# Kernel optimization log

Measured on AMD Instinct MI355X. Metric: run time of the kernel, lower is better.

## Reference

```python
import jax, jax.numpy as jnp
import numpy as np

EPS = 1e-8
MASK_MIN = 0.0


def setup_inputs() -> dict:
    key = jax.random.key(0)
    k1, k2, k3, k4 = jax.random.split(key, 4)
    B, H, CELLS, W = 8, 8, 8192, 256
    memory = jax.random.normal(k1, (B, CELLS, W), dtype=jnp.float32)
    keys = jax.random.normal(k2, (B, H, W), dtype=jnp.float32)
    betas = jax.random.uniform(k3, (B, H), dtype=jnp.float32)
    mask = jax.random.uniform(k4, (B, H, W), dtype=jnp.float32)
    return {"memory": memory, "keys": keys, "betas": betas, "mask": mask}


def reference(memory, keys, betas, mask):
    # memory: [B, C, W]; keys: [B, H, W]; betas: [B, H]; mask: [B, H, W]
    mask = mask * (1.0 - MASK_MIN) + MASK_MIN
    m2 = mask * mask                                   # [B, H, W]
    keys_m = keys * mask                               # masked keys
    # (memory*mask) . (keys*mask) summed over W == memory . (keys*mask^2)
    dots = jnp.einsum('bcw,bhw->bhc', memory, keys * m2)        # [B, H, C]
    keys_norm = jnp.linalg.norm(keys_m, axis=-1)                # [B, H]
    mem_norm = jnp.sqrt(jnp.einsum('bcw,bhw->bhc', memory * memory, m2))  # [B, H, C]
    norm = keys_norm[..., None] * mem_norm                      # [B, H, C]
    scores = dots / (norm + EPS) * betas[..., None]
    return jax.nn.softmax(scores, axis=-1)                      # [B, H, C]
```

## Files before the change

kernel.cpp:

```cpp
#include <hip/hip_runtime.h>
#include <cstdint>
#include <cmath>

#define EPS_F 1e-8f

constexpr int B = 8, H = 8, CELLS = 8192, W = 256;
constexpr int W4 = 64;
constexpr int TC = 32;
constexpr int NBLK = CELLS / TC;
constexpr int PAD = 65;

__global__ __launch_bounds__(256, 3) void ca_scores(
    const float4* __restrict__ mem4,
    const float* __restrict__ keys,
    const float* __restrict__ mask,
    const float* __restrict__ betas,
    float* __restrict__ out,
    float2* __restrict__ part)
{
    __shared__ float4 s_tile[TC * PAD];
    __shared__ float4 s_kq[H * PAD];
    __shared__ float4 s_m2[H * PAD];
    __shared__ float  s_kn[H];
    __shared__ float  s_fin[4 * H];
    __shared__ float  s_sum[4 * H];
    __shared__ float  s_sc[H][TC + 1];

    const int b = blockIdx.y, blk = blockIdx.x, t = threadIdx.x;
    const int c0 = blk * TC;
    const int lane = t & 63, wv = t >> 6;

    const int ph = t >> 5;
    const int pw = t & 31;
    const float4* __restrict__ kb4 = (const float4*)(keys + ((size_t)b * H + ph) * W);
    const float4* __restrict__ mb4 = (const float4*)(mask + ((size_t)b * H + ph) * W);
    float4 k0 = kb4[pw], k1 = kb4[pw + 32];
    float4 m0 = mb4[pw], m1 = mb4[pw + 32];

    const float4* __restrict__ gbase = mem4 + ((size_t)b * CELLS + c0) * W4;
    float4 st[8];
#pragma unroll
    for (int i = 0; i < 8; ++i) st[i] = gbase[t + i * 256];

    float4 q0 = make_float4(m0.x * m0.x, m0.y * m0.y, m0.z * m0.z, m0.w * m0.w);
    float4 q1 = make_float4(m1.x * m1.x, m1.y * m1.y, m1.z * m1.z, m1.w * m1.w);
    float4 kq0 = make_float4(k0.x * q0.x, k0.y * q0.y, k0.z * q0.z, k0.w * q0.w);
    float4 kq1 = make_float4(k1.x * q1.x, k1.y * q1.y, k1.z * q1.z, k1.w * q1.w);
    s_kq[ph * PAD + pw]      = kq0;
    s_kq[ph * PAD + pw + 32] = kq1;
    s_m2[ph * PAD + pw]      = q0;
    s_m2[ph * PAD + pw + 32] = q1;
    float km;
    float v = 0.f;
    km = k0.x * m0.x; v = fmaf(km, km, v);
    km = k0.y * m0.y; v = fmaf(km, km, v);
    km = k0.z * m0.z; v = fmaf(km, km, v);
    km = k0.w * m0.w; v = fmaf(km, km, v);
    km = k1.x * m1.x; v = fmaf(km, km, v);
    km = k1.y * m1.y; v = fmaf(km, km, v);
    km = k1.z * m1.z; v = fmaf(km, km, v);
    km = k1.w * m1.w; v = fmaf(km, km, v);
#pragma unroll
    for (int s = 1; s < 32; s <<= 1) v += __shfl_xor(v, s, 64);
    if ((t & 31) == 0) s_kn[ph] = sqrtf(v);

#pragma unroll
    for (int i = 0; i < 8; ++i) {
        int g = t + i * 256;
        s_tile[(g >> 6) * PAD + (g & 63)] = st[i];
    }
    __syncthreads();

    const int h  = lane & 7;
    const int cs = lane >> 3;
    const int c  = wv * 8 + cs;
    const float4* __restrict__ pa = s_tile + c * PAD;
    const float4* __restrict__ pk = s_kq + h * PAD;
    const float4* __restrict__ pq = s_m2 + h * PAD;

    float4 dt = make_float4(0.f, 0.f, 0.f, 0.f);
    float4 nr = make_float4(0.f, 0.f, 0.f, 0.f);
#pragma unroll 8
    for (int w = 0; w < W4; ++w) {
        float4 a  = pa[w];
        float4 kq = pk[w];
        float4 q  = pq[w];
        dt.x = fmaf(a.x, kq.x, dt.x);
        dt.y = fmaf(a.y, kq.y, dt.y);
        dt.z = fmaf(a.z, kq.z, dt.z);
        dt.w = fmaf(a.w, kq.w, dt.w);
        nr.x = fmaf(a.x * a.x, q.x, nr.x);
        nr.y = fmaf(a.y * a.y, q.y, nr.y);
        nr.z = fmaf(a.z * a.z, q.z, nr.z);
        nr.w = fmaf(a.w * a.w, q.w, nr.w);
    }
    float d = (dt.x + dt.y) + (dt.z + dt.w);
    float n = (nr.x + nr.y) + (nr.z + nr.w);

    float kn = s_kn[h];
    float be = betas[b * H + h];
    float score = d * be / (kn * sqrtf(n) + EPS_F);
    s_sc[h][c] = score;

    float mx = score;
#pragma unroll
    for (int s = 8; s < 64; s <<= 1) mx = fmaxf(mx, __shfl_xor(mx, s, 64));
    if (lane < 8) s_fin[wv * 8 + lane] = mx;
    __syncthreads();

    {
        const int oh = t >> 5, oc = t & 31;
        out[((size_t)(b * H + oh)) * CELLS + c0 + oc] = s_sc[oh][oc];
    }
    float gm = fmaxf(fmaxf(s_fin[h], s_fin[8 + h]),
                     fmaxf(s_fin[16 + h], s_fin[24 + h]));
    float e = expf(score - gm);
#pragma unroll
    for (int s = 8; s < 64; s <<= 1) e += __shfl_xor(e, s, 64);
    if (lane < 8) s_sum[wv * 8 + lane] = e;
    __syncthreads();
    if (t < 8) {
        float s4 = (s_sum[t] + s_sum[8 + t]) + (s_sum[16 + t] + s_sum[24 + t]);
        part[((size_t)(b * H + t)) * NBLK + blk] = make_float2(gm, s4);
    }
}

__global__ __launch_bounds__(256) void ca_norm(
    float* __restrict__ out, const float2* __restrict__ part)
{
    const int row = blockIdx.x >> 3;
    const int seg = blockIdx.x & 7;
    const int t = threadIdx.x, lane = t & 63;

    const float2* __restrict__ pp = part + (size_t)row * NBLK;
    float2 a0 = pp[lane], a1 = pp[lane + 64], a2 = pp[lane + 128], a3 = pp[lane + 192];
    float gm = fmaxf(fmaxf(a0.x, a1.x), fmaxf(a2.x, a3.x));
#pragma unroll
    for (int s = 32; s; s >>= 1) gm = fmaxf(gm, __shfl_xor(gm, s, 64));
    float gs = a0.y * expf(a0.x - gm) + a1.y * expf(a1.x - gm)
             + a2.y * expf(a2.x - gm) + a3.y * expf(a3.x - gm);
#pragma unroll
    for (int s = 32; s; s >>= 1) gs += __shfl_xor(gs, s, 64);
    float inv = 1.0f / gs;

    float4* p = (float4*)(out + (size_t)row * CELLS) + seg * 256;
    float4 vv = p[t];
    vv.x = expf(vv.x - gm) * inv;
    vv.y = expf(vv.y - gm) * inv;
    vv.z = expf(vv.z - gm) * inv;
    vv.w = expf(vv.w - gm) * inv;
    p[t] = vv;
}

extern "C" void kernel_launch(void* const* d_in, const int* in_sizes, int n_in,
                              void* d_out, int out_size, void* d_ws, size_t ws_size,
                              hipStream_t stream) {
    (void)in_sizes; (void)n_in; (void)out_size; (void)ws_size;
    const float* memory = (const float*)d_in[0];
    const float* keys   = (const float*)d_in[1];
    const float* betas  = (const float*)d_in[2];
    const float* mask   = (const float*)d_in[3];
    float* out = (float*)d_out;
    float2* part = (float2*)d_ws;

    dim3 gA(NBLK, B);
    ca_scores<<<gA, 256, 0, stream>>>((const float4*)memory, keys, mask, betas,
                                      out, part);
    ca_norm<<<8 * B * H, 256, 0, stream>>>(out, part);
}
```

Measured before the change: 28.27 us.

## Precompute masked keys in prep kernel and hold them in registers with DPP reductions

Adds a small prep kernel that computes keys*mask^2, mask^2, key norms and betas once per (b,h) and writes them to workspace in a lane-friendly interleaved layout. The score kernel then loads these weights straight into registers instead of rebuilding them in shared memory in every block. Each lane covers two heads and a slice of W across 8 cells, and the partial sums are reduced with DPP row rotations. This is meant to cut redundant per-block key/mask work and shared-memory reads. In exchange it adds a third kernel launch and raises register pressure to 16 float4 weights per thread.

```diff
diff --git a/kernel.cpp b/kernel.cpp
--- a/kernel.cpp
+++ b/kernel.cpp
@@ -8,121 +8,148 @@
 constexpr int W4 = 64;
 constexpr int TC = 32;
 constexpr int NBLK = CELLS / TC;
-constexpr int PAD = 65;
+
+constexpr int OFF_CB   = 32768;
+constexpr int OFF_PART = 32896;
+
+template <int CTRL>
+__device__ __forceinline__ float ror_add(float v) {
+    int x = __builtin_amdgcn_update_dpp(0, __builtin_bit_cast(int, v),
+                                        CTRL, 0xf, 0xf, false);
+    return v + __builtin_bit_cast(float, x);
+}
+__device__ __forceinline__ float row_sum16(float v) {
+    v = ror_add<0x121>(v);
+    v = ror_add<0x122>(v);
+    v = ror_add<0x124>(v);
+    v = ror_add<0x128>(v);
+    return v;
+}
+
+__global__ __launch_bounds__(256) void ca_prep(
+    const float* __restrict__ keys, const float* __restrict__ mask,
+    const float* __restrict__ betas, float* __restrict__ ws)
+{
+    const int bh = blockIdx.x;
+    const int b = bh >> 3, h = bh & 7;
+    const int t = threadIdx.x;
+    float k = keys[bh * W + t];
+    float m = mask[bh * W + t];
+    float m2 = m * m;
+    float kq = k * m2;
+
+    const int w4 = t >> 2, e = t & 3;
+    const int j = w4 >> 4, wsl = w4 & 15;
+    const int hp = h & 3, hh = h >> 2;
+    size_t base = ((((size_t)b * 64 + hp * 16 + wsl) * 16) + j * 4 + hh * 2) * 4 + e;
+    ws[base]     = kq;
+    ws[base + 4] = m2;
+
+    float km = k * m;
+    float v = km * km;
+#pragma unroll
+    for (int s = 32; s; s >>= 1) v += __shfl_xor(v, s, 64);
+    __shared__ float red[4];
+    const int lane = t & 63, wv = t >> 6;
+    if (lane == 0) red[wv] = v;
+    __syncthreads();
+    if (t == 0) {
+        float kn = sqrtf((red[0] + red[1]) + (red[2] + red[3]));
+        ((float2*)(ws + OFF_CB))[bh] = make_float2(kn, betas[bh]);
+    }
+}
 
 __global__ __launch_bounds__(256, 3) void ca_scores(
     const float4* __restrict__ mem4,
-    const float* __restrict__ keys,
-    const float* __restrict__ mask,
-    const float* __restrict__ betas,
+    const float* __restrict__ ws,
     float* __restrict__ out,
     float2* __restrict__ part)
 {
-    __shared__ float4 s_tile[TC * PAD];
-    __shared__ float4 s_kq[H * PAD];
-    __shared__ float4 s_m2[H * PAD];
-    __shared__ float  s_kn[H];
-    __shared__ float  s_fin[4 * H];
-    __shared__ float  s_sum[4 * H];
+    __shared__ float4 s_tile[TC * W4];
     __shared__ float  s_sc[H][TC + 1];
+    __shared__ float  s_fin[H], s_sum2[H];
 
     const int b = blockIdx.y, blk = blockIdx.x, t = threadIdx.x;
     const int c0 = blk * TC;
     const int lane = t & 63, wv = t >> 6;
-
-    const int ph = t >> 5;
-    const int pw = t & 31;
-    const float4* __restrict__ kb4 = (const float4*)(keys + ((size_t)b * H + ph) * W);
-    const float4* __restrict__ mb4 = (const float4*)(mask + ((size_t)b * H + ph) * W);
-    float4 k0 = kb4[pw], k1 = kb4[pw + 32];
-    float4 m0 = mb4[pw], m1 = mb4[pw + 32];
+    const int hp  = (lane >> 4) & 3;
+    const int wsl = lane & 15;
 
     const float4* __restrict__ gbase = mem4 + ((size_t)b * CELLS + c0) * W4;
     float4 st[8];
 #pragma unroll
     for (int i = 0; i < 8; ++i) st[i] = gbase[t + i * 256];
 
-    float4 q0 = make_float4(m0.x * m0.x, m0.y * m0.y, m0.z * m0.z, m0.w * m0.w);
-    float4 q1 = make_float4(m1.x * m1.x, m1.y * m1.y, m1.z * m1.z, m1.w * m1.w);
-    float4 kq0 = make_float4(k0.x * q0.x, k0.y * q0.y, k0.z * q0.z, k0.w * q0.w);
-    float4 kq1 = make_float4(k1.x * q1.x, k1.y * q1.y, k1.z * q1.z, k1.w * q1.w);
-    s_kq[ph * PAD + pw]      = kq0;
-    s_kq[ph * PAD + pw + 32] = kq1;
-    s_m2[ph * PAD + pw]      = q0;
-    s_m2[ph * PAD + pw + 32] = q1;
-    float km;
-    float v = 0.f;
-    km = k0.x * m0.x; v = fmaf(km, km, v);
-    km = k0.y * m0.y; v = fmaf(km, km, v);
-    km = k0.z * m0.z; v = fmaf(km, km, v);
-    km = k0.w * m0.w; v = fmaf(km, km, v);
-    km = k1.x * m1.x; v = fmaf(km, km, v);
-    km = k1.y * m1.y; v = fmaf(km, km, v);
-    km = k1.z * m1.z; v = fmaf(km, km, v);
-    km = k1.w * m1.w; v = fmaf(km, km, v);
+    const float4* __restrict__ tbase = (const float4*)ws + ((size_t)b * 64 + lane) * 16;
+    float4 tb[16];
 #pragma unroll
-    for (int s = 1; s < 32; s <<= 1) v += __shfl_xor(v, s, 64);
-    if ((t & 31) == 0) s_kn[ph] = sqrtf(v);
+    for (int i = 0; i < 16; ++i) tb[i] = tbase[i];
+    const float2* __restrict__ cbp = (const float2*)(ws + OFF_CB) + b * H;
+    float2 cbA = cbp[hp];
+    float2 cbB = cbp[hp + 4];
 
 #pragma unroll
-    for (int i = 0; i < 8; ++i) {
-        int g = t + i * 256;
-        s_tile[(g >> 6) * PAD + (g & 63)] = st[i];
+    for (int i = 0; i < 8; ++i) s_tile[t + i * 256] = st[i];
+    __syncthreads();
+
+#pragma unroll
+    for (int c = 0; c < 8; ++c) {
+        const int cell = wv * 8 + c;
+        const float4* __restrict__ pr = s_tile + cell * W4 + wsl;
+        float4 a0 = pr[0], a1 = pr[16], a2 = pr[32], a3 = pr[48];
+
+        float4 dA = make_float4(0.f, 0.f, 0.f, 0.f);
+        float4 nA = make_float4(0.f, 0.f, 0.f, 0.f);
+        float4 dB = make_float4(0.f, 0.f, 0.f, 0.f);
+        float4 nB = make_float4(0.f, 0.f, 0.f, 0.f);
+
+#define ACC(a, j)                                                           \
+        {                                                                   \
+            float4 sq = make_float4(a.x * a.x, a.y * a.y, a.z * a.z, a.w * a.w); \
+            float4 kqA = tb[(j) * 4 + 0], qA = tb[(j) * 4 + 1];             \
+            float4 kqB = tb[(j) * 4 + 2], qB = tb[(j) * 4 + 3];             \
+            dA.x = fmaf(a.x, kqA.x, dA.x); dA.y = fmaf(a.y, kqA.y, dA.y);   \
+            dA.z = fmaf(a.z, kqA.z, dA.z); dA.w = fmaf(a.w, kqA.w, dA.w);   \
+            nA.x = fmaf(sq.x, qA.x, nA.x); nA.y = fmaf(sq.y, qA.y, nA.y);   \
+            nA.z = fmaf(sq.z, qA.z, nA.z); nA.w = fmaf(sq.w, qA.w, nA.w);   \
+            dB.x = fmaf(a.x, kqB.x, dB.x); dB.y = fmaf(a.y, kqB.y, dB.y);   \
+            dB.z = fmaf(a.z, kqB.z, dB.z); dB.w = fmaf(a.w, kqB.w, dB.w);   \
+            nB.x = fmaf(sq.x, qB.x, nB.x); nB.y = fmaf(sq.y, qB.y, nB.y);   \
+            nB.z = fmaf(sq.z, qB.z, nB.z); nB.w = fmaf(sq.w, qB.w, nB.w);   \
+        }
+        ACC(a0, 0) ACC(a1, 1) ACC(a2, 2) ACC(a3, 3)
+#undef ACC
+
+        float d0 = (dA.x + dA.y) + (dA.z + dA.w);
+        float n0 = (nA.x + nA.y) + (nA.z + nA.w);
+        float d1 = (dB.x + dB.y) + (dB.z + dB.w);
+        float n1 = (nB.x + nB.y) + (nB.z + nB.w);
+        d0 = row_sum16(d0); n0 = row_sum16(n0);
+        d1 = row_sum16(d1); n1 = row_sum16(n1);
+
+        float s0 = d0 * cbA.y / (cbA.x * sqrtf(n0) + EPS_F);
+        float s1 = d1 * cbB.y / (cbB.x * sqrtf(n1) + EPS_F);
+        if (wsl == c) {
+            s_sc[hp][cell]     = s0;
+            s_sc[hp + 4][cell] = s1;
+        }
     }
     __syncthreads();
 
-    const int h  = lane & 7;
-    const int cs = lane >> 3;
-    const int c  = wv * 8 + cs;
-    const float4* __restrict__ pa = s_tile + c * PAD;
-    const float4* __restrict__ pk = s_kq + h * PAD;
-    const float4* __restrict__ pq = s_m2 + h * PAD;
+    const int oh = t >> 5, oc = t & 31;
+    float sc = s_sc[oh][oc];
+    out[((size_t)(b * H + oh)) * CELLS + c0 + oc] = sc;
 
-    float4 dt = make_float4(0.f, 0.f, 0.f, 0.f);
-    float4 nr = make_float4(0.f, 0.f, 0.f, 0.f);
-#pragma unroll 8
-    for (int w = 0; w < W4; ++w) {
-        float4 a  = pa[w];
-        float4 kq = pk[w];
-        float4 q  = pq[w];
-        dt.x = fmaf(a.x, kq.x, dt.x);
-        dt.y = fmaf(a.y, kq.y, dt.y);
-        dt.z = fmaf(a.z, kq.z, dt.z);
-        dt.w = fmaf(a.w, kq.w, dt.w);
-        nr.x = fmaf(a.x * a.x, q.x, nr.x);
-        nr.y = fmaf(a.y * a.y, q.y, nr.y);
-        nr.z = fmaf(a.z * a.z, q.z, nr.z);
-        nr.w = fmaf(a.w * a.w, q.w, nr.w);
-    }
-    float d = (dt.x + dt.y) + (dt.z + dt.w);
-    float n = (nr.x + nr.y) + (nr.z + nr.w);
-
-    float kn = s_kn[h];
-    float be = betas[b * H + h];
-    float score = d * be / (kn * sqrtf(n) + EPS_F);
-    s_sc[h][c] = score;
-
-    float mx = score;
+    float mx = sc;
 #pragma unroll
-    for (int s = 8; s < 64; s <<= 1) mx = fmaxf(mx, __shfl_xor(mx, s, 64));
-    if (lane < 8) s_fin[wv * 8 + lane] = mx;
+    for (int s = 1; s <= 16; s <<= 1) mx = fmaxf(mx, __shfl_xor(mx, s, 64));
+    float e = expf(sc - mx);
+#pragma unroll
+    for (int s = 1; s <= 16; s <<= 1) e += __shfl_xor(e, s, 64);
+    if (oc == 0) { s_fin[oh] = mx; s_sum2[oh] = e; }
     __syncthreads();
-
-    {
-        const int oh = t >> 5, oc = t & 31;
-        out[((size_t)(b * H + oh)) * CELLS + c0 + oc] = s_sc[oh][oc];
-    }
-    float gm = fmaxf(fmaxf(s_fin[h], s_fin[8 + h]),
-                     fmaxf(s_fin[16 + h], s_fin[24 + h]));
-    float e = expf(score - gm);
-#pragma unroll
-    for (int s = 8; s < 64; s <<= 1) e += __shfl_xor(e, s, 64);
-    if (lane < 8) s_sum[wv * 8 + lane] = e;
-    __syncthreads();
-    if (t < 8) {
-        float s4 = (s_sum[t] + s_sum[8 + t]) + (s_sum[16 + t] + s_sum[24 + t]);
-        part[((size_t)(b * H + t)) * NBLK + blk] = make_float2(gm, s4);
-    }
+    if (t < H)
+        part[((size_t)(b * H + t)) * NBLK + blk] = make_float2(s_fin[t], s_sum2[t]);
 }
 
 __global__ __launch_bounds__(256) void ca_norm(
@@ -161,10 +188,11 @@
     const float* betas  = (const float*)d_in[2];
     const float* mask   = (const float*)d_in[3];
     float* out = (float*)d_out;
-    float2* part = (float2*)d_ws;
+    float* ws  = (float*)d_ws;
+    float2* part = (float2*)(ws + OFF_PART);
 
+    ca_prep<<<B * H, 256, 0, stream>>>(keys, mask, betas, ws);
     dim3 gA(NBLK, B);
-    ca_scores<<<gA, 256, 0, stream>>>((const float4*)memory, keys, mask, betas,
-                                      out, part);
+    ca_scores<<<gA, 256, 0, stream>>>((const float4*)memory, ws, out, part);
     ca_norm<<<8 * B * H, 256, 0, stream>>>(out, part);
 }
```

New measurement: 38.59 us. 1.37x slower.
